# Kernel optimization log

Measured on AMD Instinct MI355X. Metric: run time of the kernel, lower is better.

Reference implementation:

```python
import jax, jax.numpy as jnp
import numpy as np


def _gcn_conv(x, edge_index, W, b):
    # PyG GCNConv: h = D^{-1/2} (A + I) D^{-1/2} (x @ W) + b
    n = x.shape[0]
    xw = x @ W  # [N, C]
    loop = jnp.arange(n, dtype=edge_index.dtype)
    row = jnp.concatenate([edge_index[0], loop])  # source (x_j)
    col = jnp.concatenate([edge_index[1], loop])  # target (aggregation index)
    deg = jax.ops.segment_sum(jnp.ones_like(col, dtype=xw.dtype), col, num_segments=n)
    dinv = jnp.where(deg > 0, deg ** -0.5, 0.0)
    norm = dinv[row] * dinv[col]  # [E+N]
    out = jax.ops.segment_sum(xw[row] * norm[:, None], col, num_segments=n)
    return out + b


def setup_inputs() -> dict:
    key = jax.random.key(0)
    ks = jax.random.split(key, 8)
    N, F, E = 100000, 512, 3200000
    W_SCALE = 0.1  # keep sigmoid un-saturated
    x = jax.random.normal(ks[0], (N, F), dtype=jnp.float32)
    edge_index = jax.random.randint(ks[1], (2, E), 0, N, dtype=jnp.int64)
    Wg = jax.random.normal(ks[2], (F, 16), dtype=jnp.float32) * W_SCALE
    bg = jnp.zeros((16,), dtype=jnp.float32)
    W1 = jax.random.normal(ks[3], (16, 16), dtype=jnp.float32) * W_SCALE
    b1 = jnp.zeros((16,), dtype=jnp.float32)
    W2 = jax.random.normal(ks[4], (16, 32), dtype=jnp.float32) * W_SCALE
    b2 = jnp.zeros((32,), dtype=jnp.float32)
    W3 = jax.random.normal(ks[5], (32, 1), dtype=jnp.float32) * W_SCALE
    b3 = jnp.zeros((1,), dtype=jnp.float32)
    return {"x": x, "edge_index": edge_index, "Wg": Wg, "bg": bg,
            "W1": W1, "b1": b1, "W2": W2, "b2": b2, "W3": W3, "b3": b3}


def reference(x, edge_index, Wg, bg, W1, b1, W2, b2, W3, b3):
    h = jax.nn.relu(_gcn_conv(x, edge_index, Wg, bg))
    h = jax.nn.relu(h @ W1 + b1)
    h = jax.nn.relu(h @ W2 + b2)
    return jax.nn.sigmoid(h @ W3 + b3)  # [N, 1]
```

## Files before the change

kernel.cpp:

```cpp
#include <hip/hip_runtime.h>
#include <math.h>


static constexpr int F = 512;
static constexpr int C = 16;
static constexpr int BSH = 7;
static constexpr int BSZ = 128;
static constexpr int NBMAX = 1024;
static constexpr int EPB = 16384;

__global__ __launch_bounds__(256) void k_xw_bcount(const float* __restrict__ x,
                                                   const float* __restrict__ Wg,
                                                   float* __restrict__ xw, int n,
                                                   const int* __restrict__ dst,
                                                   int* __restrict__ bh, int E, int gb)
{
    if ((int)blockIdx.x >= gb) {
        __shared__ int hist[NBMAX];
        for (int i = threadIdx.x; i < NBMAX; i += 256) hist[i] = 0;
        __syncthreads();
        int g = blockIdx.x - gb;
        int base = g * EPB;
#pragma unroll 4
        for (int j = 0; j < EPB / 256; ++j) {
            int e = base + j * 256 + threadIdx.x;
            if (e < E) atomicAdd(&hist[dst[e] >> BSH], 1);
        }
        __syncthreads();
        int* row = bh + (size_t)g * NBMAX;
        for (int i = threadIdx.x; i < NBMAX; i += 256) row[i] = hist[i];
        return;
    }
    int row = blockIdx.x * 256 + threadIdx.x;
    if (row >= n) return;
    float acc[C];
#pragma unroll
    for (int c = 0; c < C; ++c) acc[c] = 0.f;
    const float4* xr = (const float4*)(x + (size_t)row * F);
#pragma unroll 4
    for (int k4 = 0; k4 < F / 4; ++k4) {
        float4 xv = xr[k4];
        const float* w = Wg + k4 * 4 * C;
#pragma unroll
        for (int j = 0; j < 4; ++j) {
            float xs = (j == 0) ? xv.x : (j == 1) ? xv.y : (j == 2) ? xv.z : xv.w;
#pragma unroll
            for (int c = 0; c < C; ++c)
                acc[c] = fmaf(xs, w[j * C + c], acc[c]);
        }
    }
    float4* o = (float4*)(xw + (size_t)row * C);
#pragma unroll
    for (int q = 0; q < 4; ++q)
        o[q] = make_float4(acc[4 * q + 0], acc[4 * q + 1], acc[4 * q + 2], acc[4 * q + 3]);
}

__global__ __launch_bounds__(1024) void k_scan(int* __restrict__ bh,
                                               int* __restrict__ bstart, int geb)
{
    int b = threadIdx.x;
    int run = 0;
    int g = 0;
    for (; g + 16 <= geb; g += 16) {
        int v[16];
#pragma unroll
        for (int j = 0; j < 16; ++j) v[j] = bh[(size_t)(g + j) * NBMAX + b];
#pragma unroll
        for (int j = 0; j < 16; ++j) {
            bh[(size_t)(g + j) * NBMAX + b] = run;
            run += v[j];
        }
    }
    for (; g < geb; ++g) {
        size_t idx = (size_t)g * NBMAX + b;
        int v = bh[idx];
        bh[idx] = run;
        run += v;
    }
    __shared__ int sh[NBMAX];
    int v0 = run;
    sh[b] = run;
    __syncthreads();
    for (int d = 1; d < NBMAX; d <<= 1) {
        int u = (b >= d) ? sh[b - d] : 0;
        __syncthreads();
        sh[b] += u;
        __syncthreads();
    }
    bstart[b] = sh[b] - v0;
    if (b == NBMAX - 1) bstart[NBMAX] = sh[b];
}

__global__ __launch_bounds__(256) void k_bscatter(const int* __restrict__ ei,
                                                  const int* __restrict__ bh,
                                                  const int* __restrict__ bstart,
                                                  int* __restrict__ packed, int E)
{
    __shared__ int cur[NBMAX];
    int g = blockIdx.x;
    const int* row = bh + (size_t)g * NBMAX;
    for (int i = threadIdx.x; i < NBMAX; i += 256) cur[i] = bstart[i] + row[i];
    __syncthreads();
    int base = g * EPB;
#pragma unroll 2
    for (int j = 0; j < EPB / 256; ++j) {
        int e = base + j * 256 + threadIdx.x;
        if (e < E) {
            int d = ei[E + e];
            int s = ei[e];
            int b = d >> BSH;
            int r = atomicAdd(&cur[b], 1);
            packed[r] = s | ((d & (BSZ - 1)) << 17);
        }
    }
}

__global__ __launch_bounds__(256) void k_bcsr(const int* __restrict__ packed,
                                              const int* __restrict__ bstart,
                                              float* __restrict__ y,
                                              int* __restrict__ srcs,
                                              int* __restrict__ starts,
                                              int* __restrict__ cnt,
                                              float* __restrict__ dinv, int n)
{
    int b = blockIdx.x, t = threadIdx.x;
    __shared__ int hist[BSZ];
    __shared__ int sc[BSZ];
    __shared__ float sdi[BSZ];
    if (t < BSZ) hist[t] = 0;
    __syncthreads();
    int beg = bstart[b], end = bstart[b + 1];
    for (int e = beg + t; e < end; e += 256)
        atomicAdd(&hist[(packed[e] >> 17) & (BSZ - 1)], 1);
    __syncthreads();
    int myc = 0;
    if (t < BSZ) { myc = hist[t]; sc[t] = myc; }
    __syncthreads();
    for (int d = 1; d < BSZ; d <<= 1) {
        int u = 0;
        if (t < BSZ && t >= d) u = sc[t - d];
        __syncthreads();
        if (t < BSZ) sc[t] += u;
        __syncthreads();
    }
    int node0 = b << BSH;
    if (t < BSZ) {
        int lst = sc[t] - myc;
        sc[t] = lst;
        float di = rsqrtf((float)(myc + 1));
        sdi[t] = di;
        int node = node0 + t;
        if (node < n) { starts[node] = beg + lst; cnt[node] = myc; dinv[node] = di; }
        hist[t] = 0;
    }
    __syncthreads();
    for (int e = beg + t; e < end; e += 256) {
        int p = packed[e];
        int dl = (p >> 17) & (BSZ - 1);
        int r = atomicAdd(&hist[dl], 1);
        srcs[beg + sc[dl] + r] = p & 0x1FFFF;
    }
    int nn = n - node0; if (nn > BSZ) nn = BSZ;
    if (nn <= 0) return;
    int lim = nn * 4;
    float4* yv = (float4*)(y + (size_t)node0 * C);
    for (int i = t; i < lim; i += 256) {
        float di = sdi[i >> 2];
        float4 v = yv[i];
        v.x *= di; v.y *= di; v.z *= di; v.w *= di;
        yv[i] = v;
    }
}

__global__ __launch_bounds__(256) void k_gather_mlp(const float* __restrict__ y,
                                                    const int* __restrict__ srcs,
                                                    const int* __restrict__ starts,
                                                    const int* __restrict__ cnt,
                                                    const float* __restrict__ dinv,
                                                    const float* __restrict__ bg,
                                                    const float* __restrict__ W1,
                                                    const float* __restrict__ b1,
                                                    const float* __restrict__ W2,
                                                    const float* __restrict__ b2,
                                                    const float* __restrict__ W3,
                                                    const float* __restrict__ b3,
                                                    float* __restrict__ out, int n)
{
    __shared__ float sh[64][17];
    int tid = threadIdx.x;
    int gtid = blockIdx.x * 256 + tid;
    int i = gtid >> 2;
    int q = tid & 3;
    if (i < n) {
        const float4* yv = (const float4*)y;
        float4 acc = yv[(size_t)i * 4 + q];
        int beg = starts[i];
        int end = beg + cnt[i];
        int e = beg;
        int headEnd = (beg + 3) & ~3;
        if (headEnd > end) headEnd = end;
        for (; e < headEnd; ++e) {
            float4 v = yv[(size_t)srcs[e] * 4 + q];
            acc.x += v.x; acc.y += v.y; acc.z += v.z; acc.w += v.w;
        }
        for (; e + 4 <= end; e += 4) {
            int4 s4 = *(const int4*)(srcs + e);
            float4 v0 = yv[(size_t)s4.x * 4 + q];
            float4 v1 = yv[(size_t)s4.y * 4 + q];
            float4 v2 = yv[(size_t)s4.z * 4 + q];
            float4 v3 = yv[(size_t)s4.w * 4 + q];
            acc.x += v0.x + v1.x + v2.x + v3.x;
            acc.y += v0.y + v1.y + v2.y + v3.y;
            acc.z += v0.z + v1.z + v2.z + v3.z;
            acc.w += v0.w + v1.w + v2.w + v3.w;
        }
        for (; e < end; ++e) {
            float4 v = yv[(size_t)srcs[e] * 4 + q];
            acc.x += v.x; acc.y += v.y; acc.z += v.z; acc.w += v.w;
        }
        float di = dinv[i];
        const float* bq = bg + q * 4;
        int lr = tid >> 2;
        sh[lr][4 * q + 0] = fmaxf(fmaf(acc.x, di, bq[0]), 0.f);
        sh[lr][4 * q + 1] = fmaxf(fmaf(acc.y, di, bq[1]), 0.f);
        sh[lr][4 * q + 2] = fmaxf(fmaf(acc.z, di, bq[2]), 0.f);
        sh[lr][4 * q + 3] = fmaxf(fmaf(acc.w, di, bq[3]), 0.f);
    }
    __syncthreads();
    if (tid < 64) {
        int node = blockIdx.x * 64 + tid;
        if (node < n) {
            float h[16];
#pragma unroll
            for (int k = 0; k < 16; ++k) h[k] = sh[tid][k];
            float h1[16];
#pragma unroll
            for (int c = 0; c < 16; ++c) {
                float s = b1[c];
#pragma unroll
                for (int k = 0; k < 16; ++k) s = fmaf(h[k], W1[k * 16 + c], s);
                h1[c] = fmaxf(s, 0.f);
            }
            float h2[32];
#pragma unroll
            for (int c = 0; c < 32; ++c) {
                float s = b2[c];
#pragma unroll
                for (int k = 0; k < 16; ++k) s = fmaf(h1[k], W2[k * 32 + c], s);
                h2[c] = fmaxf(s, 0.f);
            }
            float s = b3[0];
#pragma unroll
            for (int k = 0; k < 32; ++k) s = fmaf(h2[k], W3[k], s);
            out[node] = 1.f / (1.f + expf(-s));
        }
    }
}

extern "C" void kernel_launch(void* const* d_in, const int* in_sizes, int n_in,
                              void* d_out, int out_size, void* d_ws, size_t ws_size,
                              hipStream_t stream)
{
    const float* x  = (const float*)d_in[0];
    const int*   ei = (const int*)d_in[1];
    const float* Wg = (const float*)d_in[2];
    const float* bg = (const float*)d_in[3];
    const float* W1 = (const float*)d_in[4];
    const float* b1 = (const float*)d_in[5];
    const float* W2 = (const float*)d_in[6];
    const float* b2 = (const float*)d_in[7];
    const float* W3 = (const float*)d_in[8];
    const float* b3 = (const float*)d_in[9];
    float* out = (float*)d_out;

    int n = in_sizes[0] / F;
    int E = in_sizes[1] / 2;

    int gb  = (n + 255) / 256;
    int geb = (E + EPB - 1) / EPB;
    int NB  = (n + BSZ - 1) >> BSH;

    char* ws = (char*)d_ws;
    size_t off = 0;
    float* y      = (float*)(ws + off); off += (size_t)n * C * sizeof(float);
    int*   packed = (int*)  (ws + off); off += (size_t)E * sizeof(int);
    int*   srcs   = (int*)  (ws + off);
    int*   bh     = srcs;
    size_t big = (size_t)E; if ((size_t)geb * NBMAX > big) big = (size_t)geb * NBMAX;
    off += big * sizeof(int);
    int*   starts = (int*)  (ws + off); off += (size_t)((n + 3) & ~3) * sizeof(int);
    int*   cnt    = (int*)  (ws + off); off += (size_t)((n + 3) & ~3) * sizeof(int);
    float* dinv   = (float*)(ws + off); off += (size_t)((n + 3) & ~3) * sizeof(float);
    int*   bstart = (int*)  (ws + off);

    k_xw_bcount<<<gb + geb, 256, 0, stream>>>(x, Wg, y, n, ei + E, bh, E, gb);
    k_scan<<<1, 1024, 0, stream>>>(bh, bstart, geb);
    k_bscatter<<<geb, 256, 0, stream>>>(ei, bh, bstart, packed, E);
    k_bcsr<<<NB, 256, 0, stream>>>(packed, bstart, y, srcs, starts, cnt, dinv, n);
    k_gather_mlp<<<(n + 63) / 64, 256, 0, stream>>>(y, srcs, starts, cnt, dinv, bg,
                                                    W1, b1, W2, b2, W3, b3, out, n);
}
```

Before: 484.0 us.

## Fuse bucket scan into scatter kernel, each block recomputes its own prefix

```diff
diff --git a/kernel.cpp b/kernel.cpp
--- a/kernel.cpp
+++ b/kernel.cpp
@@ -37,7 +37,7 @@
 #pragma unroll
     for (int c = 0; c < C; ++c) acc[c] = 0.f;
     const float4* xr = (const float4*)(x + (size_t)row * F);
-#pragma unroll 4
+#pragma unroll 8
     for (int k4 = 0; k4 < F / 4; ++k4) {
         float4 xv = xr[k4];
         const float* w = Wg + k4 * 4 * C;
@@ -55,56 +55,80 @@
         o[q] = make_float4(acc[4 * q + 0], acc[4 * q + 1], acc[4 * q + 2], acc[4 * q + 3]);
 }
 
-__global__ __launch_bounds__(1024) void k_scan(int* __restrict__ bh,
-                                               int* __restrict__ bstart, int geb)
-{
-    int b = threadIdx.x;
-    int run = 0;
-    int g = 0;
-    for (; g + 16 <= geb; g += 16) {
-        int v[16];
-#pragma unroll
-        for (int j = 0; j < 16; ++j) v[j] = bh[(size_t)(g + j) * NBMAX + b];
-#pragma unroll
-        for (int j = 0; j < 16; ++j) {
-            bh[(size_t)(g + j) * NBMAX + b] = run;
-            run += v[j];
-        }
-    }
-    for (; g < geb; ++g) {
-        size_t idx = (size_t)g * NBMAX + b;
-        int v = bh[idx];
-        bh[idx] = run;
-        run += v;
-    }
-    __shared__ int sh[NBMAX];
-    int v0 = run;
-    sh[b] = run;
-    __syncthreads();
-    for (int d = 1; d < NBMAX; d <<= 1) {
-        int u = (b >= d) ? sh[b - d] : 0;
-        __syncthreads();
-        sh[b] += u;
-        __syncthreads();
-    }
-    bstart[b] = sh[b] - v0;
-    if (b == NBMAX - 1) bstart[NBMAX] = sh[b];
-}
-
 __global__ __launch_bounds__(256) void k_bscatter(const int* __restrict__ ei,
                                                   const int* __restrict__ bh,
-                                                  const int* __restrict__ bstart,
-                                                  int* __restrict__ packed, int E)
-{
+                                                  int* __restrict__ bstart,
+                                                  int* __restrict__ packed,
+                                                  int E, int geb)
+{
+    __shared__ int s_excl[NBMAX];
     __shared__ int cur[NBMAX];
-    int g = blockIdx.x;
-    const int* row = bh + (size_t)g * NBMAX;
-    for (int i = threadIdx.x; i < NBMAX; i += 256) cur[i] = bstart[i] + row[i];
-    __syncthreads();
+    int g = blockIdx.x, t = threadIdx.x;
+
+    int own[4], tot[4];
+#pragma unroll
+    for (int k = 0; k < 4; ++k) { own[k] = 0; tot[k] = 0; }
+    int gg = 0;
+    for (; gg + 4 <= geb; gg += 4) {
+        int v[4][4];
+#pragma unroll
+        for (int j = 0; j < 4; ++j)
+#pragma unroll
+            for (int k = 0; k < 4; ++k)
+                v[j][k] = bh[(size_t)(gg + j) * NBMAX + t + 256 * k];
+#pragma unroll
+        for (int j = 0; j < 4; ++j)
+#pragma unroll
+            for (int k = 0; k < 4; ++k) {
+                if (gg + j == g) own[k] = tot[k];
+                tot[k] += v[j][k];
+            }
+    }
+    for (; gg < geb; ++gg) {
+#pragma unroll
+        for (int k = 0; k < 4; ++k) {
+            int v = bh[(size_t)gg * NBMAX + t + 256 * k];
+            if (gg == g) own[k] = tot[k];
+            tot[k] += v;
+        }
+    }
+#pragma unroll
+    for (int k = 0; k < 4; ++k) s_excl[t + 256 * k] = tot[k];
+    __syncthreads();
+
+    int c0 = s_excl[4 * t], c1 = s_excl[4 * t + 1],
+        c2 = s_excl[4 * t + 2], c3 = s_excl[4 * t + 3];
+    int csum = c0 + c1 + c2 + c3;
+    cur[t] = csum;
+    __syncthreads();
+    for (int d = 1; d < 256; d <<= 1) {
+        int u = (t >= d) ? cur[t - d] : 0;
+        __syncthreads();
+        cur[t] += u;
+        __syncthreads();
+    }
+    int chunk_excl = cur[t] - csum;
+    __syncthreads();
+
+    int e0 = chunk_excl, e1 = e0 + c0, e2 = e1 + c1, e3 = e2 + c2;
+    s_excl[4 * t] = e0; s_excl[4 * t + 1] = e1;
+    s_excl[4 * t + 2] = e2; s_excl[4 * t + 3] = e3;
+    __syncthreads();
+
+#pragma unroll
+    for (int k = 0; k < 4; ++k)
+        cur[t + 256 * k] = s_excl[t + 256 * k] + own[k];
+    if (g == 0) {
+#pragma unroll
+        for (int k = 0; k < 4; ++k) bstart[t + 256 * k] = s_excl[t + 256 * k];
+        if (t == 255) bstart[NBMAX] = e3 + c3;
+    }
+    __syncthreads();
+
     int base = g * EPB;
 #pragma unroll 2
     for (int j = 0; j < EPB / 256; ++j) {
-        int e = base + j * 256 + threadIdx.x;
+        int e = base + j * 256 + t;
         if (e < E) {
             int d = ei[E + e];
             int s = ei[e];
@@ -294,8 +318,7 @@
     int*   bstart = (int*)  (ws + off);
 
     k_xw_bcount<<<gb + geb, 256, 0, stream>>>(x, Wg, y, n, ei + E, bh, E, gb);
-    k_scan<<<1, 1024, 0, stream>>>(bh, bstart, geb);
-    k_bscatter<<<geb, 256, 0, stream>>>(ei, bh, bstart, packed, E);
+    k_bscatter<<<geb, 256, 0, stream>>>(ei, bh, bstart, packed, E, geb);
     k_bcsr<<<NB, 256, 0, stream>>>(packed, bstart, y, srcs, starts, cnt, dinv, n);
     k_gather_mlp<<<(n + 63) / 64, 256, 0, stream>>>(y, srcs, starts, cnt, dinv, bg,
                                                     W1, b1, W2, b2, W3, b3, out, n);
```

Result: no change. 484.9 us (+0.2%).
